# Kernel optimization log

Hardware: AMD Instinct MI355X
Metric: run time of the kernel (lower is better)

The kernel has to match this reference:

```python
import jax, jax.numpy as jnp
import numpy as np

N_SRC = 100000
N_DST = 100000
N_EDGES = 640000
D = 128
D_OUT = 128


def setup_inputs() -> dict:
    key = jax.random.key(0)
    k1, k2, k3, k4, k5, k6 = jax.random.split(key, 6)
    h_src = jax.random.normal(k1, (N_SRC, D), dtype=jnp.float32)
    h_dst = jax.random.normal(k2, (N_DST, D), dtype=jnp.float32)
    src_idx = jax.random.randint(k3, (N_EDGES,), 0, N_SRC, dtype=jnp.int32)
    dst_idx = jax.random.randint(k4, (N_EDGES,), 0, N_DST, dtype=jnp.int32)
    W = jax.random.normal(k5, (2 * D, D_OUT), dtype=jnp.float32) * 0.05
    b = jax.random.normal(k6, (D_OUT,), dtype=jnp.float32) * 0.05
    return {"h_src": h_src, "h_dst": h_dst, "src_idx": src_idx,
            "dst_idx": dst_idx, "W": W, "b": b}


def reference(h_src, h_dst, src_idx, dst_idx, W, b):
    # copy_u: gather source features along edges -> [E, D]
    msgs = h_src[src_idx]
    # mean aggregation per destination node (segment mean)
    summed = jax.ops.segment_sum(msgs, dst_idx, num_segments=N_DST)  # [N_dst, D]
    deg = jax.ops.segment_sum(jnp.ones((N_EDGES,), dtype=h_src.dtype),
                              dst_idx, num_segments=N_DST)  # [N_dst]
    h_N = summed / jnp.maximum(deg, 1.0)[:, None]
    # concat self + neighbor mean, then linear projection
    h_total = jnp.concatenate([h_dst, h_N], axis=1)  # [N_dst, 2D]
    return h_total @ W + b
```

## Files before the change

### kernel.cpp

```cpp
#include <hip/hip_runtime.h>

#define D 128
#define N_SRC 100000
#define N_DST 100000
#define N_EDGES 640000

#define SCAN_BLK 1024
#define N_SCAN_BLOCKS ((N_DST + SCAN_BLK - 1) / SCAN_BLK)

#define HIST_BLOCKS ((N_EDGES + 255) / 256)
#define CVT_BLOCKS  ((N_SRC * D / 8) / 256)
#define PACKW_BLOCKS 128

typedef __attribute__((ext_vector_type(8))) short s8v;
typedef __attribute__((ext_vector_type(4))) float f32x4;

__device__ __forceinline__ unsigned short f2bf(float f) {
    unsigned int u = __float_as_uint(f);
    u += 0x7fffu + ((u >> 16) & 1u);
    return (unsigned short)(u >> 16);
}

__device__ __forceinline__ unsigned int pk2(float a, float b) {
    return (unsigned int)f2bf(a) | ((unsigned int)f2bf(b) << 16);
}

__global__ __launch_bounds__(256) void prep(
    const int* __restrict__ dst_idx, int* __restrict__ counts,
    const float* __restrict__ h_src, unsigned int* __restrict__ A32,
    const float* __restrict__ W, unsigned short* __restrict__ Bp)
{
    const int blk = blockIdx.x;
    const int tid = threadIdx.x;
    if (blk < HIST_BLOCKS) {
        int e = blk * 256 + tid;
        if (e < N_EDGES) atomicAdd(&counts[dst_idx[e]], 1);
    } else if (blk < HIST_BLOCKS + CVT_BLOCKS) {
        int id = (blk - HIST_BLOCKS) * 256 + tid;
        size_t e = (size_t)id * 8;
        const float4* p = (const float4*)(h_src + e);
        float4 x = p[0], y = p[1];
        uint4 o;
        o.x = pk2(x.x, x.y); o.y = pk2(x.z, x.w);
        o.z = pk2(y.x, y.y); o.w = pk2(y.z, y.w);
        int r = id >> 4;
        int c = (id & 15) * 8;
        *(uint4*)(A32 + (size_t)r * 128 + (c >> 1)) = o;
    } else {
        int id = (blk - HIST_BLOCKS - CVT_BLOCKS) * 256 + tid;
        if (id < 32768) {
            int j = id & 7;
            int l = (id >> 3) & 63;
            int t = (id >> 9) & 7;
            int s = id >> 12;
            int k = s * 32 + (l >> 4) * 8 + j;
            int n = t * 16 + (l & 15);
            Bp[id] = f2bf(W[k * D + n]);
        }
    }
}


__global__ __launch_bounds__(256) void scan_blocks(
    const int* __restrict__ counts, int* __restrict__ row_start,
    int* __restrict__ block_sums)
{
    __shared__ int sh[256];
    const int tid = threadIdx.x;
    const int base = blockIdx.x * SCAN_BLK + tid * 4;
    int v[4];
    int local = 0;
#pragma unroll
    for (int k = 0; k < 4; k++) {
        int idx = base + k;
        v[k] = (idx < N_DST) ? counts[idx] : 0;
        local += v[k];
    }
    sh[tid] = local;
    __syncthreads();
    for (int off = 1; off < 256; off <<= 1) {
        int t = (tid >= off) ? sh[tid - off] : 0;
        __syncthreads();
        sh[tid] += t;
        __syncthreads();
    }
    int run = (tid == 0) ? 0 : sh[tid - 1];
    if (tid == 255) block_sums[blockIdx.x] = sh[255];
#pragma unroll
    for (int k = 0; k < 4; k++) {
        int idx = base + k;
        if (idx < N_DST) row_start[idx] = run;
        run += v[k];
    }
}

__global__ __launch_bounds__(256) void add_offsets(
    int* __restrict__ row_start, const int* __restrict__ block_sums,
    int* __restrict__ cursor)
{
    __shared__ int sh[128];
    const int tid = threadIdx.x;
    if (tid < 128) sh[tid] = (tid < N_SCAN_BLOCKS) ? block_sums[tid] : 0;
    __syncthreads();
    for (int off = 1; off < 128; off <<= 1) {
        int t = (tid < 128 && tid >= off) ? sh[tid - off] : 0;
        __syncthreads();
        if (tid < 128) sh[tid] += t;
        __syncthreads();
    }
    int i = blockIdx.x * 256 + tid;
    if (i < N_DST) {
        int blk = i / SCAN_BLK;
        int off = (blk == 0) ? 0 : sh[blk - 1];
        int v = row_start[i] + off;
        row_start[i] = v;
        cursor[i] = v;
    }
    if (i == 0) row_start[N_DST] = N_EDGES;
}

__global__ __launch_bounds__(256) void scatter_perm(
    const int* __restrict__ src_idx, const int* __restrict__ dst_idx,
    int* __restrict__ cursor, int* __restrict__ edge_src)
{
    int e = blockIdx.x * 256 + threadIdx.x;
    if (e < N_EDGES) {
        int d = dst_idx[e];
        int pos = atomicAdd(&cursor[d], 1);
        edge_src[pos] = src_idx[e];
    }
}

__global__ __launch_bounds__(256) void aggregate(
    const unsigned short* __restrict__ hs16,
    const int* __restrict__ row_start,
    const int* __restrict__ edge_src, unsigned int* __restrict__ A32)
{
    const int wave = threadIdx.x >> 6;
    const int grp = (threadIdx.x >> 4) & 3;
    const int gl = threadIdx.x & 15;
    const int row = blockIdx.x * 16 + wave * 4 + grp;
    const int start = row_start[row];
    const int deg = row_start[row + 1] - start;
    float acc[8] = {0.f, 0.f, 0.f, 0.f, 0.f, 0.f, 0.f, 0.f};
    for (int base = 0; base < deg; base += 8) {
        int j = base + (gl & 7);
        int myid = edge_src[start + min(j, deg - 1)];
#pragma unroll
        for (int t = 0; t < 8; t++) {
            int s = __shfl(myid, t, 16);
            uint4 u = *(const uint4*)(hs16 + (size_t)s * 256 + gl * 8);
            float m = ((base + t) < deg) ? 1.f : 0.f;
            acc[0] = fmaf(__uint_as_float(u.x << 16), m, acc[0]);
            acc[1] = fmaf(__uint_as_float(u.x & 0xffff0000u), m, acc[1]);
            acc[2] = fmaf(__uint_as_float(u.y << 16), m, acc[2]);
            acc[3] = fmaf(__uint_as_float(u.y & 0xffff0000u), m, acc[3]);
            acc[4] = fmaf(__uint_as_float(u.z << 16), m, acc[4]);
            acc[5] = fmaf(__uint_as_float(u.z & 0xffff0000u), m, acc[5]);
            acc[6] = fmaf(__uint_as_float(u.w << 16), m, acc[6]);
            acc[7] = fmaf(__uint_as_float(u.w & 0xffff0000u), m, acc[7]);
        }
    }
    const float inv = 1.0f / fmaxf((float)deg, 1.0f);
    uint4 o;
    o.x = pk2(acc[0] * inv, acc[1] * inv);
    o.y = pk2(acc[2] * inv, acc[3] * inv);
    o.z = pk2(acc[4] * inv, acc[5] * inv);
    o.w = pk2(acc[6] * inv, acc[7] * inv);
    *(uint4*)(A32 + (size_t)row * 128 + 64 + gl * 4) = o;
}

__global__ __launch_bounds__(256, 3) void mfma_gemm(
    const float* __restrict__ h_dst,
    const unsigned short* __restrict__ A,
    const unsigned short* __restrict__ Bp,
    const float* __restrict__ bias,
    float* __restrict__ out)
{
    const int wave = threadIdx.x >> 6;
    const int lane = threadIdx.x & 63;
    const int quad = lane >> 4;
    const int lr = lane & 15;
    const int row0 = blockIdx.x * 64;
    const int t0 = wave * 2;

    s8v Bf[8][2];
#pragma unroll
    for (int s = 0; s < 8; s++)
#pragma unroll
        for (int j = 0; j < 2; j++)
            Bf[s][j] = *(const s8v*)(Bp + ((size_t)(s * 8 + t0 + j) * 64 + lane) * 8);

    f32x4 acc[4][2];
#pragma unroll
    for (int rg = 0; rg < 4; rg++)
#pragma unroll
        for (int j = 0; j < 2; j++)
            acc[rg][j] = (f32x4){0.f, 0.f, 0.f, 0.f};

#pragma unroll
    for (int rg = 0; rg < 4; rg++) {
        int r = row0 + rg * 16 + lr;
        int rc = min(r, N_DST - 1);
        const float* p = h_dst + (size_t)rc * D + quad * 8;
        const unsigned short* q = A + (size_t)rc * 256 + 128 + quad * 8;

        float4 x[4], y[4];
        s8v an[4];
#pragma unroll
        for (int s = 0; s < 4; s++) {
            x[s] = *(const float4*)(p + s * 32);
            y[s] = *(const float4*)(p + s * 32 + 4);
            an[s] = *(const s8v*)(q + s * 32);
        }
#pragma unroll
        for (int s = 0; s < 8; s++) {
            s8v a0;
            if (s < 4) {
                unsigned short au[8];
                au[0] = f2bf(x[s].x); au[1] = f2bf(x[s].y);
                au[2] = f2bf(x[s].z); au[3] = f2bf(x[s].w);
                au[4] = f2bf(y[s].x); au[5] = f2bf(y[s].y);
                au[6] = f2bf(y[s].z); au[7] = f2bf(y[s].w);
                a0 = *(s8v*)au;
            } else {
                a0 = an[s - 4];
            }
            acc[rg][0] = __builtin_amdgcn_mfma_f32_16x16x32_bf16(a0, Bf[s][0], acc[rg][0], 0, 0, 0);
            acc[rg][1] = __builtin_amdgcn_mfma_f32_16x16x32_bf16(a0, Bf[s][1], acc[rg][1], 0, 0, 0);
        }
    }

    __syncthreads();

    float bv0 = bias[t0 * 16 + lr];
    float bv1 = bias[(t0 + 1) * 16 + lr];
#pragma unroll
    for (int rg = 0; rg < 4; rg++) {
#pragma unroll
        for (int r = 0; r < 4; r++) {
            int row = row0 + rg * 16 + quad * 4 + r;
            if (row < N_DST) {
                out[(size_t)row * D + t0 * 16 + lr] = acc[rg][0][r] + bv0;
                out[(size_t)row * D + (t0 + 1) * 16 + lr] = acc[rg][1][r] + bv1;
            }
        }
    }
}

extern "C" void kernel_launch(void* const* d_in, const int* in_sizes, int n_in,
                              void* d_out, int out_size, void* d_ws, size_t ws_size,
                              hipStream_t stream) {
    const float* h_src  = (const float*)d_in[0];
    const float* h_dst  = (const float*)d_in[1];
    const int* src_idx  = (const int*)d_in[2];
    const int* dst_idx  = (const int*)d_in[3];
    const float* W      = (const float*)d_in[4];
    const float* b      = (const float*)d_in[5];
    float* out = (float*)d_out;

    unsigned short* Bp = (unsigned short*)d_ws;
    int* ws_i          = (int*)((char*)d_ws + 65536);
    int* row_start     = ws_i;
    int* cursor        = row_start + (N_DST + 1);
    int* counts        = cursor + N_DST;
    int* block_sums    = counts + N_DST;
    int* edge_src      = block_sums + N_SCAN_BLOCKS;

    hipMemsetAsync(counts, 0, (size_t)N_DST * sizeof(int), stream);

    prep<<<HIST_BLOCKS + CVT_BLOCKS + PACKW_BLOCKS, 256, 0, stream>>>(
        dst_idx, counts, h_src, (unsigned int*)d_out, W, Bp);

    scan_blocks<<<N_SCAN_BLOCKS, 256, 0, stream>>>(counts, row_start, block_sums);
    add_offsets<<<(N_DST + 255) / 256, 256, 0, stream>>>(row_start, block_sums, cursor);
    scatter_perm<<<(N_EDGES + 255) / 256, 256, 0, stream>>>(src_idx, dst_idx, cursor, edge_src);

    aggregate<<<N_DST / 16, 256, 0, stream>>>(
        (const unsigned short*)d_out, row_start, edge_src, (unsigned int*)d_out);

    int gemm_blocks = (N_DST + 63) / 64;
    mfma_gemm<<<gemm_blocks, 256, 0, stream>>>(
        h_dst, (const unsigned short*)d_out, Bp, b, out);
}
```

Baseline: 279.3 us.

## Restructure GEMM so each wave computes full output width with B staged in LDS

The GEMM kernel now processes 128 rows per block, with each wave owning 32 rows across all 128 output columns, instead of each wave owning 2 column tiles over 64 rows. The packed bf16 weight matrix is staged through shared memory in two halves rather than held as per-wave register fragments loaded from global. This reduces redundant A-row loads and bf16 conversions across waves and halves the block count. In exchange it adds more accumulator registers (launch bounds lowered to 2), extra LDS reads and barriers.

```diff
diff --git a/kernel.cpp b/kernel.cpp
--- a/kernel.cpp
+++ b/kernel.cpp
@@ -170,80 +170,108 @@
     *(uint4*)(A32 + (size_t)row * 128 + 64 + gl * 4) = o;
 }
 
-__global__ __launch_bounds__(256, 3) void mfma_gemm(
+__global__ __launch_bounds__(256, 2) void mfma_gemm(
     const float* __restrict__ h_dst,
     const unsigned short* __restrict__ A,
     const unsigned short* __restrict__ Bp,
     const float* __restrict__ bias,
     float* __restrict__ out)
 {
-    const int wave = threadIdx.x >> 6;
-    const int lane = threadIdx.x & 63;
+    __shared__ uint4 Bs4[2048];
+    unsigned short* Bs = (unsigned short*)Bs4;
+    const int tid = threadIdx.x;
+    const int wave = tid >> 6;
+    const int lane = tid & 63;
     const int quad = lane >> 4;
     const int lr = lane & 15;
-    const int row0 = blockIdx.x * 64;
-    const int t0 = wave * 2;
-
-    s8v Bf[8][2];
-#pragma unroll
-    for (int s = 0; s < 8; s++)
-#pragma unroll
-        for (int j = 0; j < 2; j++)
-            Bf[s][j] = *(const s8v*)(Bp + ((size_t)(s * 8 + t0 + j) * 64 + lane) * 8);
-
-    f32x4 acc[4][2];
-#pragma unroll
-    for (int rg = 0; rg < 4; rg++)
-#pragma unroll
-        for (int j = 0; j < 2; j++)
-            acc[rg][j] = (f32x4){0.f, 0.f, 0.f, 0.f};
-
-#pragma unroll
-    for (int rg = 0; rg < 4; rg++) {
-        int r = row0 + rg * 16 + lr;
-        int rc = min(r, N_DST - 1);
-        const float* p = h_dst + (size_t)rc * D + quad * 8;
-        const unsigned short* q = A + (size_t)rc * 256 + 128 + quad * 8;
-
-        float4 x[4], y[4];
-        s8v an[4];
-#pragma unroll
-        for (int s = 0; s < 4; s++) {
-            x[s] = *(const float4*)(p + s * 32);
-            y[s] = *(const float4*)(p + s * 32 + 4);
-            an[s] = *(const s8v*)(q + s * 32);
-        }
-#pragma unroll
-        for (int s = 0; s < 8; s++) {
-            s8v a0;
-            if (s < 4) {
-                unsigned short au[8];
-                au[0] = f2bf(x[s].x); au[1] = f2bf(x[s].y);
-                au[2] = f2bf(x[s].z); au[3] = f2bf(x[s].w);
-                au[4] = f2bf(y[s].x); au[5] = f2bf(y[s].y);
-                au[6] = f2bf(y[s].z); au[7] = f2bf(y[s].w);
-                a0 = *(s8v*)au;
-            } else {
-                a0 = an[s - 4];
-            }
-            acc[rg][0] = __builtin_amdgcn_mfma_f32_16x16x32_bf16(a0, Bf[s][0], acc[rg][0], 0, 0, 0);
-            acc[rg][1] = __builtin_amdgcn_mfma_f32_16x16x32_bf16(a0, Bf[s][1], acc[rg][1], 0, 0, 0);
-        }
-    }
-
-    __syncthreads();
-
-    float bv0 = bias[t0 * 16 + lr];
-    float bv1 = bias[(t0 + 1) * 16 + lr];
-#pragma unroll
-    for (int rg = 0; rg < 4; rg++) {
+    const int row0 = blockIdx.x * 128 + wave * 32;
+
+    const int r0 = min(row0 + lr, N_DST - 1);
+    const int r1 = min(row0 + 16 + lr, N_DST - 1);
+
+    {
+        const uint4* src = (const uint4*)Bp;
+#pragma unroll
+        for (int i = 0; i < 8; i++)
+            Bs4[tid + i * 256] = src[tid + i * 256];
+    }
+
+    const float* p0 = h_dst + (size_t)r0 * D + quad * 8;
+    const float* p1 = h_dst + (size_t)r1 * D + quad * 8;
+    const unsigned short* q0 = A + (size_t)r0 * 256 + 128 + quad * 8;
+    const unsigned short* q1 = A + (size_t)r1 * 256 + 128 + quad * 8;
+
+    float4 x0[4], y0[4], x1[4], y1[4];
+    s8v an0[4], an1[4];
+#pragma unroll
+    for (int s = 0; s < 4; s++) {
+        x0[s] = *(const float4*)(p0 + s * 32);
+        y0[s] = *(const float4*)(p0 + s * 32 + 4);
+        x1[s] = *(const float4*)(p1 + s * 32);
+        y1[s] = *(const float4*)(p1 + s * 32 + 4);
+        an0[s] = *(const s8v*)(q0 + s * 32);
+        an1[s] = *(const s8v*)(q1 + s * 32);
+    }
+    s8v af0[4], af1[4];
+#pragma unroll
+    for (int s = 0; s < 4; s++) {
+        unsigned short u0[8], u1[8];
+        u0[0]=f2bf(x0[s].x); u0[1]=f2bf(x0[s].y); u0[2]=f2bf(x0[s].z); u0[3]=f2bf(x0[s].w);
+        u0[4]=f2bf(y0[s].x); u0[5]=f2bf(y0[s].y); u0[6]=f2bf(y0[s].z); u0[7]=f2bf(y0[s].w);
+        u1[0]=f2bf(x1[s].x); u1[1]=f2bf(x1[s].y); u1[2]=f2bf(x1[s].z); u1[3]=f2bf(x1[s].w);
+        u1[4]=f2bf(y1[s].x); u1[5]=f2bf(y1[s].y); u1[6]=f2bf(y1[s].z); u1[7]=f2bf(y1[s].w);
+        af0[s] = *(s8v*)u0;
+        af1[s] = *(s8v*)u1;
+    }
+
+    f32x4 acc0[8], acc1[8];
+#pragma unroll
+    for (int t = 0; t < 8; t++) {
+        acc0[t] = (f32x4){0.f, 0.f, 0.f, 0.f};
+        acc1[t] = (f32x4){0.f, 0.f, 0.f, 0.f};
+    }
+
+    __syncthreads();
+
+#pragma unroll
+    for (int s = 0; s < 4; s++) {
+#pragma unroll
+        for (int t = 0; t < 8; t++) {
+            s8v bf = *(const s8v*)(Bs + ((s * 8 + t) * 64 + lane) * 8);
+            acc0[t] = __builtin_amdgcn_mfma_f32_16x16x32_bf16(af0[s], bf, acc0[t], 0, 0, 0);
+            acc1[t] = __builtin_amdgcn_mfma_f32_16x16x32_bf16(af1[s], bf, acc1[t], 0, 0, 0);
+        }
+    }
+
+    __syncthreads();
+
+    {
+        const uint4* src = (const uint4*)(Bp + 16384);
+#pragma unroll
+        for (int i = 0; i < 8; i++)
+            Bs4[tid + i * 256] = src[tid + i * 256];
+    }
+    __syncthreads();
+
+#pragma unroll
+    for (int s = 0; s < 4; s++) {
+#pragma unroll
+        for (int t = 0; t < 8; t++) {
+            s8v bf = *(const s8v*)(Bs + ((s * 8 + t) * 64 + lane) * 8);
+            acc0[t] = __builtin_amdgcn_mfma_f32_16x16x32_bf16(an0[s], bf, acc0[t], 0, 0, 0);
+            acc1[t] = __builtin_amdgcn_mfma_f32_16x16x32_bf16(an1[s], bf, acc1[t], 0, 0, 0);
+        }
+    }
+
+#pragma unroll
+    for (int t = 0; t < 8; t++) {
+        float bv = bias[t * 16 + lr];
 #pragma unroll
         for (int r = 0; r < 4; r++) {
-            int row = row0 + rg * 16 + quad * 4 + r;
-            if (row < N_DST) {
-                out[(size_t)row * D + t0 * 16 + lr] = acc[rg][0][r] + bv0;
-                out[(size_t)row * D + (t0 + 1) * 16 + lr] = acc[rg][1][r] + bv1;
-            }
+            int rowa = row0 + quad * 4 + r;
+            int rowb = row0 + 16 + quad * 4 + r;
+            if (rowa < N_DST) out[(size_t)rowa * D + t * 16 + lr] = acc0[t][r] + bv;
+            if (rowb < N_DST) out[(size_t)rowb * D + t * 16 + lr] = acc1[t][r] + bv;
         }
     }
 }
@@ -279,7 +307,7 @@
     aggregate<<<N_DST / 16, 256, 0, stream>>>(
         (const unsigned short*)d_out, row_start, edge_src, (unsigned int*)d_out);
 
-    int gemm_blocks = (N_DST + 63) / 64;
+    int gemm_blocks = (N_DST + 127) / 128;
     mfma_gemm<<<gemm_blocks, 256, 0, stream>>>(
         h_dst, (const unsigned short*)d_out, Bp, b, out);
 }
```

Result: faster. 264.4 us (-5.3%).
